# Performance work log

Measured on AMD Instinct MI355X. Metric: run time of the kernel, lower is better.

## Reference

```python
import jax, jax.numpy as jnp
import numpy as np

B, N, H, S = 64, 2048, 128, 8192
K, DEAD_K = 32, 8
BN_EPS = 1e-5


def _bn_train(x, gamma, beta):
    # BatchNorm1d training-mode math over (batch, length) per channel; x: [B,C,N]
    mean = jnp.mean(x, axis=(0, 2), keepdims=True)
    var = jnp.var(x, axis=(0, 2), keepdims=True)
    xh = (x - mean) * jax.lax.rsqrt(var + BN_EPS)
    return xh * gamma[None, :, None] + beta[None, :, None]


def setup_inputs() -> dict:
    key = jax.random.key(0)
    ks = jax.random.split(key, 20)

    def lin(k, out_d, in_d):
        s = 1.0 / np.sqrt(in_d)
        return jax.random.uniform(k, (out_d, in_d), jnp.float32, -s, s)

    def bias(k, d, fan_in):
        s = 1.0 / np.sqrt(fan_in)
        return jax.random.uniform(k, (d,), jnp.float32, -s, s)

    inp = {
        "pts": jax.random.normal(ks[0], (B, 3, N), jnp.float32),
        "dead_features": jax.random.randint(ks[1], (S,), 0, 10, jnp.int32),
        "conv1_w": lin(ks[2], 128, 3), "conv1_b": bias(ks[3], 128, 3),
        "conv2_w": lin(ks[4], 128, 128), "conv2_b": bias(ks[5], 128, 128),
        "conv3_w": lin(ks[6], 256, 128), "conv3_b": bias(ks[7], 256, 128),
        "conv4_w": lin(ks[8], 512, 256), "conv4_b": bias(ks[9], 512, 256),
        "bn1_g": jnp.ones(128), "bn1_b": jnp.zeros(128),
        "bn2_g": jnp.ones(128), "bn2_b": jnp.zeros(128),
        "bn3_g": jnp.ones(256), "bn3_b": jnp.zeros(256),
        "bn4_g": jnp.ones(512), "bn4_b": jnp.zeros(512),
        "fc1_w": lin(ks[10], 256, 512), "fc1_b": bias(ks[11], 256, 512),
        "fc2_w": lin(ks[12], H, 256), "fc2_b": bias(ks[13], H, 256),
        "sae2_w": lin(ks[14], H, S),  # sae1.weight = sae2.weight.T (tied init)
        "sae1_b": jnp.zeros(S), "sae2_b": jnp.zeros(H),
    }
    inp["sae1_w"] = inp["sae2_w"].T  # [S,H]
    return inp


def reference(pts, dead_features, conv1_w, conv1_b, conv2_w, conv2_b,
              conv3_w, conv3_b, conv4_w, conv4_b,
              bn1_g, bn1_b, bn2_g, bn2_b, bn3_g, bn3_b, bn4_g, bn4_b,
              fc1_w, fc1_b, fc2_w, fc2_b, sae2_w, sae1_b, sae2_b, sae1_w):
    def conv1x1(x, w, b):  # x:[B,Ci,N] w:[Co,Ci] -> [B,Co,N]
        return jnp.einsum('bcn,oc->bon', x, w) + b[None, :, None]

    h = jax.nn.relu(_bn_train(conv1x1(pts, conv1_w, conv1_b), bn1_g, bn1_b))
    h = jax.nn.relu(_bn_train(conv1x1(h, conv2_w, conv2_b), bn2_g, bn2_b))
    h = jax.nn.relu(_bn_train(conv1x1(h, conv3_w, conv3_b), bn3_g, bn3_b))
    h = _bn_train(conv1x1(h, conv4_w, conv4_b), bn4_g, bn4_b)
    h = jnp.max(h, axis=2)  # global max pool -> [B,512]
    h = jax.nn.relu(h @ fc1_w.T + fc1_b)
    x = jax.nn.relu(h @ fc2_w.T + fc2_b)  # hidden rep [B,H]

    # run_sae (stage 1, batch_topk=True)
    _x = x - sae2_b
    f = jax.nn.relu(_x @ sae1_w.T + sae1_b)  # [B,S]
    flat = f.reshape(-1)                     # [B*S]
    topk_vals, inds = jax.lax.top_k(flat, K * B)
    dead_mask = jnp.broadcast_to(dead_features >= 5, (B, S)).reshape(-1)
    dead_flat = jnp.where(dead_mask, flat, 0.0)
    dead_vals, dead_inds = jax.lax.top_k(dead_flat, DEAD_K * B)
    f_out = jnp.zeros_like(flat).at[inds].set(topk_vals).reshape(B, S)
    dead_f = jnp.zeros_like(flat).at[dead_inds].set(dead_vals).reshape(B, S)
    recon = f_out @ sae2_w.T + sae2_b
    dead_x = dead_f @ sae2_w.T + sae2_b
    return (x, recon, f_out, dead_x)
```

## Files before the change

kernel.cpp:

```cpp
#include <hip/hip_runtime.h>
#include <hip/hip_bf16.h>
#include <stdint.h>

#define B_   64
#define N_   2048
#define C1_  128
#define C2_  128
#define C3_  256
#define C4_  512
#define H_   128
#define S_   8192
#define KTOT 2048
#define DTOT 512
#define TIE_CAP 4096
#define BN_EPS 1e-5f
#define NPART 1024

#define I_PTS 0
#define I_DEAD 1
#define I_C1W 2
#define I_C1B 3
#define I_C2W 4
#define I_C2B 5
#define I_C3W 6
#define I_C3B 7
#define I_C4W 8
#define I_C4B 9
#define I_BN1G 10
#define I_BN1B 11
#define I_BN2G 12
#define I_BN2B 13
#define I_BN3G 14
#define I_BN3B 15
#define I_BN4G 16
#define I_BN4B 17
#define I_FC1W 18
#define I_FC1B 19
#define I_FC2W 20
#define I_FC2B 21
#define I_SAE2W 22
#define I_SAE1B 23
#define I_SAE2B 24
#define I_SAE1W 25

typedef const void* const* Tbl;
struct P26 { const void* p[26]; };

typedef _Float16 f16x8 __attribute__((ext_vector_type(8)));
typedef float f32x16 __attribute__((ext_vector_type(16)));

typedef const __attribute__((address_space(1))) uint32_t* gas_t;
typedef __attribute__((address_space(3))) uint32_t* las_t;
#define GLL(g, s) __builtin_amdgcn_global_load_lds((gas_t)(const void*)(g), (las_t)(void*)(s), 16, 0, 0)

__global__ void k_sentinel(float* outx, float v){
  if(threadIdx.x==0) outx[0] = v;
}

__global__ void k_route(P26 in, const void** tbl, int* flag){
  if(threadIdx.x != 0) return;
  const uint32_t* a   = (const uint32_t*)in.p[1];
  const uint32_t* g10 = (const uint32_t*)in.p[10];
  const uint32_t* d16 = (const uint32_t*)in.p[16];
  bool onesA  = a[0]==0x3F800000u && a[1]==0x3F800000u && a[2]==0x3F800000u && a[3]==0x3F800000u;
  bool intsA  = a[0]<=9u && a[1]<=9u && a[2]<=9u && a[3]<=9u;
  bool ones10 = g10[0]==0x3F800000u && g10[1]==0x3F800000u;
  bool ints16 = d16[0]<=9u && d16[1]<=9u;
  int f = 0;
  if(intsA && ones10) f = 1;
  else if(onesA && ints16) f = 2;
  const int permI[26] = {0,1,2,3,4,5,6,7,8,9,10,11,12,13,14,15,16,17,18,19,20,21,22,23,24,25};
  const int permA[26] = {21,16,9,8,11,10,13,12,15,14,1,0,3,2,5,4,7,6,18,17,20,19,25,22,24,23};
  const int* pm = (f==2) ? permA : permI;
  for(int i=0;i<26;i++) tbl[i] = in.p[pm[i]];
  *flag = f;
}

__global__ void k_init(uint32_t* ctrl, uint32_t* cnt, uint32_t* hist,
                       uint32_t* ctrl2, uint32_t* cnt2, uint32_t* hist2,
                       float* racc, float* dacc){
  int t = blockIdx.x*256 + threadIdx.x;
  if(t < 256){ hist[t]=0u; hist2[t]=0u; }
  if(t == 0){
    ctrl[0]=0u;  ctrl[1]=KTOT;  cnt[0]=0u;  cnt[1]=0u;  cnt[2]=0u;
    ctrl2[0]=0u; ctrl2[1]=DTOT; cnt2[0]=0u; cnt2[1]=0u; cnt2[2]=0u;
  }
  if(t < B_*H_){ racc[t]=0.f; dacc[t]=0.f; }
}

__global__ void k_mom(Tbl tbl, float* __restrict__ mom){
  const float* pts = (const float*)tbl[I_PTS];
  int b = blockIdx.x, t = threadIdx.x;
  const float* p0 = pts + (size_t)b*3*N_;
  const float* p1 = p0 + N_;
  const float* p2 = p1 + N_;
  float v[9] = {};
  for(int n=t;n<N_;n+=256){
    float a=p0[n], c=p1[n], d=p2[n];
    v[0]+=a; v[1]+=c; v[2]+=d;
    v[3]=fmaf(a,a,v[3]); v[4]=fmaf(a,c,v[4]); v[5]=fmaf(a,d,v[5]);
    v[6]=fmaf(c,c,v[6]); v[7]=fmaf(c,d,v[7]); v[8]=fmaf(d,d,v[8]);
  }
  __shared__ float red[256];
  for(int i=0;i<9;i++){
    red[t]=v[i]; __syncthreads();
    for(int off=128;off>0;off>>=1){ if(t<off) red[t]+=red[t+off]; __syncthreads(); }
    if(t==0) mom[b*16+i]=red[0];
    __syncthreads();
  }
}

__global__ void k_bn1fold(const float* __restrict__ mom, Tbl tbl, float* __restrict__ ew){
  const float* w1 = (const float*)tbl[I_C1W];
  const float* b1 = (const float*)tbl[I_C1B];
  const float* g  = (const float*)tbl[I_BN1G];
  const float* be = (const float*)tbl[I_BN1B];
  __shared__ float tot[9];
  int t = threadIdx.x;
  if(t < 9){
    float s=0.f;
    for(int b=0;b<B_;b++) s += mom[b*16+t];
    tot[t]=s;
  }
  __syncthreads();
  const float inv = 1.f/((float)B_*(float)N_);
  float mu0=tot[0]*inv, mu1=tot[1]*inv, mu2=tot[2]*inv;
  float M00=tot[3]*inv, M01=tot[4]*inv, M02=tot[5]*inv;
  float M11=tot[6]*inv, M12=tot[7]*inv, M22=tot[8]*inv;
  float w0=w1[t*3+0], ww1=w1[t*3+1], w2=w1[t*3+2];
  float bb=b1[t];
  float wmu = w0*mu0 + ww1*mu1 + w2*mu2;
  float m = wmu + bb;
  float E2 = w0*w0*M00 + ww1*ww1*M11 + w2*w2*M22
           + 2.f*(w0*ww1*M01 + w0*w2*M02 + ww1*w2*M12)
           + 2.f*bb*wmu + bb*bb;
  float var = E2 - m*m; if(var<0.f) var=0.f;
  float a = g[t] / sqrtf(var + BN_EPS);
  float sh = be[t] - m*a;
  ew[t*4+0]=a*w0; ew[t*4+1]=a*ww1; ew[t*4+2]=a*w2; ew[t*4+3]=fmaf(a,bb,sh);
}

template<int CI, int CO, int SRCP, int STOREY, int MM, int TILED>
__global__ __launch_bounds__(256)
void k_conv(const float* __restrict__ yin, Tbl tbl, int wi, int bi,
            const float* __restrict__ aAct, const float* __restrict__ bAct,
            float* __restrict__ yout,
            float* __restrict__ psum, float* __restrict__ psq,
            float* __restrict__ pmx, float* __restrict__ pmn){
  const float* W    = (const float*)tbl[wi];
  const float* bias = (const float*)tbl[bi];
  __shared__ float Ws[16][132];
  __shared__ float As[16][132];
  __shared__ float ps[3][128];
  const int b  = blockIdx.z;
  const int o0 = blockIdx.y*128;
  const int n0 = blockIdx.x*128;
  const int nt = blockIdx.x;
  const int t  = threadIdx.x;
  const int tx = t & 15, ty = t >> 4;
  const int wo = t >> 1;
  const int wk = (t & 1)*8;
  const int ar = t >> 4;
  const int an4 = (t & 15)*4;
  if(SRCP){
    const float* pts = (const float*)tbl[I_PTS];
    if(t < 48){
      int j = t >> 4, cc = (t & 15)*8;
      const float* pp = pts + ((size_t)b*3 + j)*N_ + n0 + cc;
      const float4 p0 = *(const float4*)pp;
      const float4 p1 = *(const float4*)(pp+4);
      ps[j][cc+0]=p0.x; ps[j][cc+1]=p0.y; ps[j][cc+2]=p0.z; ps[j][cc+3]=p0.w;
      ps[j][cc+4]=p1.x; ps[j][cc+5]=p1.y; ps[j][cc+6]=p1.z; ps[j][cc+7]=p1.w;
    }
    __syncthreads();
  }
  const float* ybase = SRCP ? (const float*)nullptr : (yin + (size_t)b*CI*N_);
  float acc[8][8] = {};
  for(int k0=0;k0<CI;k0+=16){
    {
      const float* wp = W + (size_t)(o0+wo)*CI + (k0+wk);
      const float4 wa = *(const float4*)wp;
      const float4 wb = *(const float4*)(wp+4);
      Ws[wk+0][wo]=wa.x; Ws[wk+1][wo]=wa.y; Ws[wk+2][wo]=wa.z; Ws[wk+3][wo]=wa.w;
      Ws[wk+4][wo]=wb.x; Ws[wk+5][wo]=wb.y; Ws[wk+6][wo]=wb.z; Ws[wk+7][wo]=wb.w;
    }
    {
      const int c = k0 + ar;
      float av[8];
      if(SRCP){
        const float e0=aAct[c*4+0], e1=aAct[c*4+1], e2=aAct[c*4+2], e3=aAct[c*4+3];
        #pragma unroll
        for(int x=0;x<4;x++){
          float v = fmaf(e0, ps[0][an4+x], fmaf(e1, ps[1][an4+x], fmaf(e2, ps[2][an4+x], e3)));
          av[x] = fmaxf(v, 0.f);
        }
        #pragma unroll
        for(int x=0;x<4;x++){
          float v = fmaf(e0, ps[0][64+an4+x], fmaf(e1, ps[1][64+an4+x], fmaf(e2, ps[2][64+an4+x], e3)));
          av[4+x] = fmaxf(v, 0.f);
        }
      } else {
        const float* yp = ybase + (size_t)c*N_ + n0;
        const float4 v0 = *(const float4*)(yp + an4);
        const float4 v1 = *(const float4*)(yp + 64 + an4);
        const float a = aAct[c], bb = bAct[c];
        av[0]=fmaxf(fmaf(a,v0.x,bb),0.f); av[1]=fmaxf(fmaf(a,v0.y,bb),0.f);
        av[2]=fmaxf(fmaf(a,v0.z,bb),0.f); av[3]=fmaxf(fmaf(a,v0.w,bb),0.f);
        av[4]=fmaxf(fmaf(a,v1.x,bb),0.f); av[5]=fmaxf(fmaf(a,v1.y,bb),0.f);
        av[6]=fmaxf(fmaf(a,v1.z,bb),0.f); av[7]=fmaxf(fmaf(a,v1.w,bb),0.f);
      }
      *(float4*)&As[ar][an4]    = make_float4(av[0],av[1],av[2],av[3]);
      *(float4*)&As[ar][64+an4] = make_float4(av[4],av[5],av[6],av[7]);
    }
    __syncthreads();
    #pragma unroll
    for(int kk=0;kk<16;kk++){
      const float4 w0 = *(const float4*)&Ws[kk][ty*8];
      const float4 w1 = *(const float4*)&Ws[kk][ty*8+4];
      const float4 a0 = *(const float4*)&As[kk][tx*4];
      const float4 a1 = *(const float4*)&As[kk][64+tx*4];
      const float wr[8] = {w0.x,w0.y,w0.z,w0.w,w1.x,w1.y,w1.z,w1.w};
      const float ac[8] = {a0.x,a0.y,a0.z,a0.w,a1.x,a1.y,a1.z,a1.w};
      #pragma unroll
      for(int i=0;i<8;i++)
        #pragma unroll
        for(int j=0;j<8;j++)
          acc[i][j] = fmaf(wr[i], ac[j], acc[i][j]);
    }
    __syncthreads();
  }
  float bo[8];
  #pragma unroll
  for(int i=0;i<8;i++) bo[i] = bias[o0 + ty*8 + i];
  if(STOREY && TILED){
    const int ks = (o0 + ty*8) >> 4;
    float* yb2 = yout + ((((size_t)(b*16 + nt))*16 + ks)*128)*16 + (ty&1)*8;
    #pragma unroll
    for(int jj=0;jj<8;jj++){
      const int nn = (jj<4) ? (tx*4 + jj) : (64 + tx*4 + (jj-4));
      float4 lo = make_float4(acc[0][jj]+bo[0], acc[1][jj]+bo[1],
                              acc[2][jj]+bo[2], acc[3][jj]+bo[3]);
      float4 hi = make_float4(acc[4][jj]+bo[4], acc[5][jj]+bo[5],
                              acc[6][jj]+bo[6], acc[7][jj]+bo[7]);
      *(float4*)(yb2 + (size_t)nn*16)     = lo;
      *(float4*)(yb2 + (size_t)nn*16 + 4) = hi;
    }
  }
  #pragma unroll
  for(int i=0;i<8;i++){
    const int o = o0 + ty*8 + i;
    float v[8];
    #pragma unroll
    for(int j=0;j<8;j++) v[j] = acc[i][j] + bo[i];
    if(STOREY && !TILED){
      float* yo = yout + ((size_t)b*CO + o)*N_ + n0;
      *(float4*)(yo + tx*4)      = make_float4(v[0],v[1],v[2],v[3]);
      *(float4*)(yo + 64 + tx*4) = make_float4(v[4],v[5],v[6],v[7]);
    }
    float s = 0.f, q = 0.f;
    #pragma unroll
    for(int j=0;j<8;j++){ s += v[j]; q = fmaf(v[j],v[j],q); }
    float mx=0.f, mn=0.f;
    if(MM){
      mx = v[0]; mn = v[0];
      #pragma unroll
      for(int j=1;j<8;j++){ mx = fmaxf(mx,v[j]); mn = fminf(mn,v[j]); }
    }
    #pragma unroll
    for(int m=1;m<16;m<<=1){
      s += __shfl_xor(s,m);
      q += __shfl_xor(q,m);
      if(MM){ mx = fmaxf(mx,__shfl_xor(mx,m)); mn = fminf(mn,__shfl_xor(mn,m)); }
    }
    if(tx==0){
      psum[(size_t)o*NPART + b*16 + nt] = s;
      psq [(size_t)o*NPART + b*16 + nt] = q;
      if(MM){
        pmx[((size_t)b*CO + o)*16 + nt] = mx;
        pmn[((size_t)b*CO + o)*16 + nt] = mn;
      }
    }
  }
}

__global__ void k_wcvt(Tbl tbl, _Float16* __restrict__ whi, _Float16* __restrict__ wlo){
  const float* W = (const float*)tbl[I_C4W];
  int u = blockIdx.x*256 + threadIdx.x;
  int h = u & 1, o_loc = (u>>1)&127, ks = (u>>8)&15, oy = u>>12;
  int o = oy*128 + o_loc;
  int c0 = ks*16 + h*8;
  const float* wp = W + (size_t)o*C3_ + c0;
  f16x8 vh, vl;
  #pragma unroll
  for(int j=0;j<8;j++){
    float w = wp[j]*1024.f;
    _Float16 hi = (_Float16)w;
    vh[j] = hi;
    vl[j] = (_Float16)(w - (float)hi);
  }
  *(f16x8*)(whi + (size_t)u*8) = vh;
  *(f16x8*)(wlo + (size_t)u*8) = vl;
}

__global__ void k_t3(const float* __restrict__ y3t, const float* __restrict__ a3,
                     const float* __restrict__ b3, _Float16* __restrict__ a4){
  int u = blockIdx.x*256 + threadIdx.x;
  int h = u & 1, ks = (u>>8)&15;
  int c0 = ks*16 + h*8;
  const float* yp = y3t + (size_t)u*8;
  f16x8 vh;
  #pragma unroll
  for(int j=0;j<8;j++){
    float v = fmaxf(fmaf(a3[c0+j], yp[j], b3[c0+j]), 0.f);
    vh[j] = (_Float16)v;
  }
  *(f16x8*)(a4 + (size_t)u*8) = vh;
}

__global__ __launch_bounds__(256)
void k_conv4m(const _Float16* __restrict__ a4,
              const _Float16* __restrict__ whi, const _Float16* __restrict__ wlo,
              Tbl tbl,
              float* __restrict__ psum, float* __restrict__ psq,
              float* __restrict__ pmx, float* __restrict__ pmn){
  const float* bias = (const float*)tbl[I_C4B];
  __shared__ __align__(16) char smem[73728];
  const int nt = blockIdx.x, oy = blockIdx.y, b = blockIdx.z;
  const int t = threadIdx.x, l = t & 63, w = t >> 6;
  const int wr = w >> 1, wc = w & 1, h = l >> 5, ln = l & 31;
  const char* gWh = (const char*)whi + (size_t)oy*65536;
  const char* gWl = (const char*)wlo + (size_t)oy*65536;
  const char* gA  = (const char*)a4  + (size_t)(b*16 + nt)*65536;
  const int lo16 = l*16;
  const int aoff0 = (wr*64 +  0 + ln)*32 + h*16;
  const int aoff1 = (wr*64 + 32 + ln)*32 + h*16;
  const int boff0 = (wc*64 +  0 + ln)*32 + h*16;
  const int boff1 = (wc*64 + 32 + ln)*32 + h*16;
  f32x16 acc00 = {}, acc01 = {}, acc10 = {}, acc11 = {};

  auto stage = [&](int buf, int step){
    char* sb = smem + buf*24576;
    const size_t go = (size_t)step*8192;
    #pragma unroll
    for(int i=0;i<2;i++){
      const int off = i*4096 + w*1024;
      GLL(gWh + go + off + lo16, sb         + off);
      GLL(gWl + go + off + lo16, sb + 8192  + off);
      GLL(gA  + go + off + lo16, sb + 16384 + off);
    }
  };

  stage(0, 0);
  stage(1, 1);
  #pragma unroll
  for(int s=0; s<8; s++){
    if(s < 7){ asm volatile("s_waitcnt vmcnt(6)" ::: "memory"); }
    else     { asm volatile("s_waitcnt vmcnt(0)" ::: "memory"); }
    __builtin_amdgcn_s_barrier();
    if(s < 6) stage((s+2)%3, s+2);
    const char* sb = smem + (s%3)*24576;
    __builtin_amdgcn_s_setprio(1);
    #pragma unroll
    for(int g=0; g<2; g++){
      const char* pg = sb + g*4096;
      f16x8 ah0 = *(const f16x8*)(pg + aoff0);
      f16x8 ah1 = *(const f16x8*)(pg + aoff1);
      f16x8 al0 = *(const f16x8*)(pg + 8192 + aoff0);
      f16x8 al1 = *(const f16x8*)(pg + 8192 + aoff1);
      f16x8 b0  = *(const f16x8*)(pg + 16384 + boff0);
      f16x8 b1  = *(const f16x8*)(pg + 16384 + boff1);
      acc00 = __builtin_amdgcn_mfma_f32_32x32x16_f16(ah0, b0, acc00, 0,0,0);
      acc00 = __builtin_amdgcn_mfma_f32_32x32x16_f16(al0, b0, acc00, 0,0,0);
      acc01 = __builtin_amdgcn_mfma_f32_32x32x16_f16(ah0, b1, acc01, 0,0,0);
      acc01 = __builtin_amdgcn_mfma_f32_32x32x16_f16(al0, b1, acc01, 0,0,0);
      acc10 = __builtin_amdgcn_mfma_f32_32x32x16_f16(ah1, b0, acc10, 0,0,0);
      acc10 = __builtin_amdgcn_mfma_f32_32x32x16_f16(al1, b0, acc10, 0,0,0);
      acc11 = __builtin_amdgcn_mfma_f32_32x32x16_f16(ah1, b1, acc11, 0,0,0);
      acc11 = __builtin_amdgcn_mfma_f32_32x32x16_f16(al1, b1, acc11, 0,0,0);
    }
    __builtin_amdgcn_s_setprio(0);
  }
  __syncthreads();
  float* Ss = (float*)smem;
  float* Sq = Ss + 1024;
  float* Sx = Sq + 1024;
  float* Sn = Sx + 1024;
  const float inv = 1.f/1024.f;
  const int o0 = oy*128;
  const int grp = ln >> 3;
  #pragma unroll
  for(int to=0; to<2; to++){
    const f32x16 a0 = to ? acc10 : acc00;
    const f32x16 a1 = to ? acc11 : acc01;
    #pragma unroll
    for(int r=0; r<16; r++){
      const int row = (r&3) + 8*(r>>2) + 4*h;
      const int ol = wr*64 + to*32 + row;
      const float bo = bias[o0 + ol];
      float v0 = fmaf(a0[r], inv, bo);
      float v1 = fmaf(a1[r], inv, bo);
      float s = v0 + v1;
      float q = fmaf(v0, v0, v1*v1);
      float mx = fmaxf(v0, v1), mn = fminf(v0, v1);
      #pragma unroll
      for(int m=1; m<8; m<<=1){
        s += __shfl_xor(s, m);
        q += __shfl_xor(q, m);
        mx = fmaxf(mx, __shfl_xor(mx, m));
        mn = fminf(mn, __shfl_xor(mn, m));
      }
      if((ln & 7) == 0){
        const int idx = (wc*4 + grp)*128 + ol;
        Ss[idx] = s;  Sq[idx] = q;
        Sx[idx] = mx; Sn[idx] = mn;
      }
    }
  }
  __syncthreads();
  if(t < 128){
    const int o = o0 + t;
    float s = 0.f, q = 0.f;
    float mx = -__builtin_inff(), mn = __builtin_inff();
    #pragma unroll
    for(int g=0; g<8; g++){
      s += Ss[g*128 + t];
      q += Sq[g*128 + t];
      mx = fmaxf(mx, Sx[g*128 + t]);
      mn = fminf(mn, Sn[g*128 + t]);
    }
    psum[(size_t)o*NPART + b*16 + nt] = s;
    psq [(size_t)o*NPART + b*16 + nt] = q;
    pmx[((size_t)b*C4_ + o)*16 + nt] = mx;
    pmn[((size_t)b*C4_ + o)*16 + nt] = mn;
  }
}

__global__ void k_finalize(const float* __restrict__ psum, const float* __restrict__ psq,
                           Tbl tbl, int gi, int bi,
                           float* __restrict__ aout, float* __restrict__ bout){
  const float* gamma = (const float*)tbl[gi];
  const float* beta  = (const float*)tbl[bi];
  int c = blockIdx.x, t = threadIdx.x;
  float s=0.f, q=0.f;
  for(int i=t;i<NPART;i+=256){ s+=psum[(size_t)c*NPART+i]; q+=psq[(size_t)c*NPART+i]; }
  __shared__ float ls[256], lq[256];
  ls[t]=s; lq[t]=q; __syncthreads();
  for(int off=128; off>0; off>>=1){
    if(t<off){ ls[t]+=ls[t+off]; lq[t]+=lq[t+off]; }
    __syncthreads();
  }
  if(t==0){
    const float cnt = (float)B_*(float)N_;
    float mean = ls[0]/cnt;
    float var  = lq[0]/cnt - mean*mean;
    if(var < 0.f) var = 0.f;
    float a = gamma[c] / sqrtf(var + BN_EPS);
    aout[c] = a;
    bout[c] = beta[c] - mean*a;
  }
}

__global__ void k_pool(const float* __restrict__ pmx, const float* __restrict__ pmn,
                       const float* __restrict__ aA, const float* __restrict__ bA,
                       float* __restrict__ pooled){
  int idx = blockIdx.x*256 + threadIdx.x;
  int o = idx & (C4_-1);
  float mx=-__builtin_inff(), mn=__builtin_inff();
  for(int k=0;k<16;k++){
    mx = fmaxf(mx, pmx[(size_t)idx*16+k]);
    mn = fminf(mn, pmn[(size_t)idx*16+k]);
  }
  float a=aA[o], bb=bA[o];
  pooled[idx] = (a>=0.f) ? fmaf(a,mx,bb) : fmaf(a,mn,bb);
}

__global__ void k_fc1(const float* __restrict__ pooled, Tbl tbl, float* __restrict__ out){
  const float* w    = (const float*)tbl[I_FC1W];
  const float* bias = (const float*)tbl[I_FC1B];
  __shared__ float xp[512];
  int b = blockIdx.x, t = threadIdx.x;
  for(int i=t;i<512;i+=256) xp[i] = pooled[(size_t)b*512+i];
  __syncthreads();
  const float* wr = w + (size_t)t*512;
  float acc = 0.f;
  for(int c=0;c<512;c++) acc = fmaf(xp[c], wr[c], acc);
  out[(size_t)b*256 + t] = fmaxf(acc + bias[t], 0.f);
}

__global__ void k_fc2(const float* __restrict__ in, Tbl tbl,
                      float* __restrict__ xbuf, float* __restrict__ xout){
  const float* w    = (const float*)tbl[I_FC2W];
  const float* bias = (const float*)tbl[I_FC2B];
  __shared__ float xp[256];
  int b = blockIdx.x, t = threadIdx.x;
  for(int i=t;i<256;i+=128) xp[i] = in[(size_t)b*256+i];
  __syncthreads();
  const float* wr = w + (size_t)t*256;
  float acc = 0.f;
  for(int c=0;c<256;c++) acc = fmaf(xp[c], wr[c], acc);
  float v = fmaxf(acc + bias[t], 0.f);
  xbuf[(size_t)b*H_ + t] = v;
  xout[(size_t)b*H_ + t] = v;
}

__global__ void k_sae(const float* __restrict__ xbuf, Tbl tbl, float* __restrict__ f){
  const float* w  = (const float*)tbl[I_SAE1W];
  const float* b1 = (const float*)tbl[I_SAE1B];
  const float* b2 = (const float*)tbl[I_SAE2B];
  __shared__ float xp[H_];
  int b = blockIdx.y, t = threadIdx.x;
  if(t < H_) xp[t] = xbuf[(size_t)b*H_ + t] - b2[t];
  __syncthreads();
  int s = blockIdx.x*256 + t;
  const float* wr = w + (size_t)s*H_;
  float acc = 0.f;
  for(int h=0;h<H_;h++) acc = fmaf(xp[h], wr[h], acc);
  acc += b1[s];
  f[(size_t)b*S_ + s] = fmaxf(acc, 0.f);
}

__global__ void k_hist(const float* __restrict__ f, Tbl tbl,
                       int mode, int shift, const uint32_t* __restrict__ ctrl,
                       uint32_t* __restrict__ hist){
  const int* df = (const int*)tbl[I_DEAD];
  __shared__ uint32_t lh[256];
  int t = threadIdx.x;
  lh[t] = 0u; __syncthreads();
  const uint32_t prefix = ctrl[0];
  const uint32_t mask = (shift == 24) ? 0u : (0xFFFFFFFFu << (shift+8));
  int i0 = blockIdx.x*1024 + t;
  #pragma unroll
  for(int j=0;j<4;j++){
    int i = i0 + j*256;
    float v = f[i];
    if(mode){ int s = i & (S_-1); if(df[s] < 5) v = 0.f; }
    uint32_t u = __float_as_uint(v);
    if((u & mask) == prefix) atomicAdd(&lh[(u>>shift)&255u], 1u);
  }
  __syncthreads();
  if(lh[t]) atomicAdd(&hist[t], lh[t]);
}

__global__ void k_scan(uint32_t* ctrl, uint32_t* hist, int shift){
  if(threadIdx.x == 0){
    uint32_t rem = ctrl[1];
    uint32_t cum = 0; int tb = 0;
    for(int bin=255; bin>=0; bin--){
      uint32_t c = hist[bin];
      if(cum + c >= rem){ tb = bin; rem = rem - cum; break; }
      cum += c;
    }
    ctrl[0] |= ((uint32_t)tb) << shift;
    ctrl[1] = rem;
  }
  __syncthreads();
  hist[threadIdx.x] = 0u;
}

__global__ void k_select(const float* __restrict__ f, Tbl tbl,
                         int mode, int kcap, const uint32_t* __restrict__ ctrl,
                         uint32_t* __restrict__ cnt, uint32_t* __restrict__ sel,
                         uint32_t* __restrict__ tie){
  const int* df = (const int*)tbl[I_DEAD];
  int i = blockIdx.x*256 + threadIdx.x;
  float v = f[i];
  if(mode){ int s = i & (S_-1); if(df[s] < 5) v = 0.f; }
  uint32_t u = __float_as_uint(v);
  const uint32_t T = ctrl[0];
  if(u > T){ uint32_t p = atomicAdd(&cnt[0], 1u); if(p < (uint32_t)kcap) sel[p] = (uint32_t)i; }
  else if(u == T){ uint32_t p = atomicAdd(&cnt[1], 1u); if(p < TIE_CAP) tie[p] = (uint32_t)i; }
}

__global__ void k_resolve(const uint32_t* __restrict__ ctrl, uint32_t* __restrict__ cnt,
                          uint32_t* __restrict__ sel, const uint32_t* __restrict__ tie,
                          int kcap){
  if(threadIdx.x != 0) return;
  uint32_t m = ctrl[1];
  uint32_t ngt = cnt[0]; if(ngt > (uint32_t)kcap) ngt = (uint32_t)kcap;
  uint32_t ntie = cnt[1]; if(ntie > TIE_CAP) ntie = TIE_CAP;
  uint32_t last = 0u; bool first = true;
  for(uint32_t it=0; it<m; it++){
    uint32_t best = 0xFFFFFFFFu;
    for(uint32_t j=0;j<ntie;j++){
      uint32_t v = tie[j];
      if((first || v > last) && v < best) best = v;
    }
    if(best == 0xFFFFFFFFu) break;
    if(ngt + it < (uint32_t)kcap) sel[ngt + it] = best;
    last = best; first = false;
  }
  uint32_t tot = ngt + m; if(tot > (uint32_t)kcap) tot = (uint32_t)kcap;
  cnt[2] = tot;
}

__global__ void k_scatter(const uint32_t* __restrict__ sel, const uint32_t* __restrict__ cnt,
                          const float* __restrict__ f, float* __restrict__ fout){
  uint32_t t = blockIdx.x*256 + threadIdx.x;
  if(t >= cnt[2]) return;
  uint32_t i = sel[t];
  if(i < (uint32_t)(B_*S_)) fout[i] = f[i];
}

__global__ void k_accum(const uint32_t* __restrict__ sel, const uint32_t* __restrict__ cnt,
                        const float* __restrict__ f, Tbl tbl, int mode,
                        float* __restrict__ acc){
  const int* df = (const int*)tbl[I_DEAD];
  const float* w2 = (const float*)tbl[I_SAE2W];
  uint32_t e = blockIdx.x;
  if(e >= cnt[2]) return;
  uint32_t i = sel[e];
  if(i >= (uint32_t)(B_*S_)) return;
  uint32_t b = i >> 13, s = i & (S_-1);
  float v = f[i];
  if(mode && df[s] < 5) v = 0.f;
  int h = threadIdx.x;
  float wv = w2[(size_t)h*S_ + s];
  atomicAdd(&acc[b*H_ + h], v*wv);
}

__global__ void k_final(const float* __restrict__ racc, const float* __restrict__ dacc,
                        Tbl tbl, float* __restrict__ outR, float* __restrict__ outD){
  const float* b2 = (const float*)tbl[I_SAE2B];
  int idx = blockIdx.x*256 + threadIdx.x;
  int h = idx & (H_-1);
  float bb = b2[h];
  outR[idx] = racc[idx] + bb;
  outD[idx] = dacc[idx] + bb;
}

__global__ void k_health(const int* __restrict__ flag, const float* __restrict__ xb,
                         float* __restrict__ outx){
  __shared__ float red[256];
  int t = threadIdx.x;
  float s = 0.f;
  for(int i=t;i<B_*H_;i+=256) s += fabsf(xb[i]);
  red[t]=s; __syncthreads();
  for(int off=128;off>0;off>>=1){ if(t<off) red[t]+=red[t+off]; __syncthreads(); }
  if(t==0){
    float avg = red[0]/(float)(B_*H_);
    int f = *flag;
    float v = 0.f;
    if(f == 0) v = 12000.f;
    else if(!(avg >= 0.05f && avg <= 50.f)) v = 40000.f + 1000.f*(float)f;
    if(v > 0.f) outx[0] = v;
  }
}

extern "C" void kernel_launch(void* const* d_in, const int* in_sizes, int n_in,
                              void* d_out, int out_size, void* d_ws, size_t ws_size,
                              hipStream_t stream){
  (void)in_sizes; (void)n_in;
  float* out       = (float*)d_out;
  float* out_x     = out;
  float* out_recon = out + 8192;
  float* out_fout  = out + 16384;
  float* out_deadx = out + 540672;

  char* p = (char*)d_ws;
  auto take = [&](size_t bytes)->char*{
    char* r = p; p += (bytes + 255) & ~(size_t)255; return r;
  };
  float* y2   = (float*)take((size_t)B_*C2_*N_*4);
  float* y3   = (float*)take((size_t)B_*C3_*N_*4);
  float* psum = (float*)take((size_t)C4_*NPART*4);
  float* psq  = (float*)take((size_t)C4_*NPART*4);
  float* pmx  = (float*)take((size_t)B_*C4_*16*4);
  float* pmn  = (float*)take((size_t)B_*C4_*16*4);
  float* mom  = (float*)take(64*16*4);
  float* ab   = (float*)take(4096*4);
  float* pooled=(float*)take((size_t)B_*C4_*4);
  float* fc1o = (float*)take((size_t)B_*256*4);
  float* xb   = (float*)take((size_t)B_*H_*4);
  float* fb   = (float*)take((size_t)B_*S_*4);
  float* racc = (float*)take((size_t)B_*H_*4);
  float* dacc = (float*)take((size_t)B_*H_*4);
  uint32_t* hist  = (uint32_t*)take(256*4);
  uint32_t* ctrl  = (uint32_t*)take(64);
  uint32_t* cnt   = (uint32_t*)take(64);
  uint32_t* sel   = (uint32_t*)take((size_t)KTOT*4);
  uint32_t* tie   = (uint32_t*)take((size_t)TIE_CAP*4);
  uint32_t* hist2 = (uint32_t*)take(256*4);
  uint32_t* ctrl2 = (uint32_t*)take(64);
  uint32_t* cnt2  = (uint32_t*)take(64);
  uint32_t* sel2  = (uint32_t*)take((size_t)DTOT*4);
  uint32_t* tie2  = (uint32_t*)take((size_t)TIE_CAP*4);
  const void** tbl = (const void**)take(32*sizeof(void*));
  int* flag = (int*)take(64);
  size_t need = (size_t)(p - (char*)d_ws);
  _Float16* a4   = (_Float16*)y2;
  _Float16* w4hi = (_Float16*)fb;
  _Float16* w4lo = (_Float16*)((char*)fb + 262144);

  hipMemsetAsync(d_out, 0, (size_t)out_size*sizeof(float), stream);
  if(ws_size != 0 && ws_size < need){
    k_sentinel<<<1,64,0,stream>>>(out_x, 15000.f);
    return;
  }

  P26 ptrs;
  for(int i=0;i<26;i++) ptrs.p[i] = d_in[i];
  k_route<<<1,64,0,stream>>>(ptrs, tbl, flag);
  k_init<<<32,256,0,stream>>>(ctrl,cnt,hist,ctrl2,cnt2,hist2,racc,dacc);

  k_mom<<<B_,256,0,stream>>>(tbl,mom);
  k_bn1fold<<<1,128,0,stream>>>(mom,tbl,ab);
  k_wcvt<<<64,256,0,stream>>>(tbl, w4hi, w4lo);

  k_conv<C1_,C2_,1,1,0,0><<<dim3(N_/128,C2_/128,B_),256,0,stream>>>(
      nullptr,tbl,I_C2W,I_C2B,ab,nullptr,y2,psum,psq,nullptr,nullptr);
  k_finalize<<<C2_,256,0,stream>>>(psum,psq,tbl,I_BN2G,I_BN2B,ab+512,ab+640);
  k_conv<C2_,C3_,0,1,0,1><<<dim3(N_/128,C3_/128,B_),256,0,stream>>>(
      y2,tbl,I_C3W,I_C3B,ab+512,ab+640,y3,psum,psq,nullptr,nullptr);
  k_finalize<<<C3_,256,0,stream>>>(psum,psq,tbl,I_BN3G,I_BN3B,ab+768,ab+1024);
  k_t3<<<16384,256,0,stream>>>(y3, ab+768, ab+1024, a4);
  k_conv4m<<<dim3(16,4,64),256,0,stream>>>(a4, w4hi, w4lo, tbl,
                                           psum, psq, pmx, pmn);
  k_finalize<<<C4_,256,0,stream>>>(psum,psq,tbl,I_BN4G,I_BN4B,ab+1280,ab+1792);
  k_pool<<<(B_*C4_)/256,256,0,stream>>>(pmx,pmn,ab+1280,ab+1792,pooled);

  k_fc1<<<B_,256,0,stream>>>(pooled,tbl,fc1o);
  k_fc2<<<B_,128,0,stream>>>(fc1o,tbl,xb,out_x);
  k_sae<<<dim3(S_/256,B_),256,0,stream>>>(xb,tbl,fb);

  for(int pass=0;pass<4;pass++){
    int shift = 24 - 8*pass;
    k_hist<<<512,256,0,stream>>>(fb,tbl,0,shift,ctrl,hist);
    k_scan<<<1,256,0,stream>>>(ctrl,hist,shift);
  }
  k_select<<<2048,256,0,stream>>>(fb,tbl,0,KTOT,ctrl,cnt,sel,tie);
  k_resolve<<<1,64,0,stream>>>(ctrl,cnt,sel,tie,KTOT);
  k_scatter<<<8,256,0,stream>>>(sel,cnt,fb,out_fout);
  k_accum<<<KTOT,128,0,stream>>>(sel,cnt,fb,tbl,0,racc);

  for(int pass=0;pass<4;pass++){
    int shift = 24 - 8*pass;
    k_hist<<<512,256,0,stream>>>(fb,tbl,1,shift,ctrl2,hist2);
    k_scan<<<1,256,0,stream>>>(ctrl2,hist2,shift);
  }
  k_select<<<2048,256,0,stream>>>(fb,tbl,1,DTOT,ctrl2,cnt2,sel2,tie2);
  k_resolve<<<1,64,0,stream>>>(ctrl2,cnt2,sel2,tie2,DTOT);
  k_accum<<<DTOT,128,0,stream>>>(sel2,cnt2,fb,tbl,1,dacc);

  k_final<<<(B_*H_)/256,256,0,stream>>>(racc,dacc,tbl,out_recon,out_deadx);

  k_health<<<1,256,0,stream>>>(flag,xb,out_x);
}
```

Measured before the change: 718.0 us.

## Load conv4 MFMA fragments directly from global with fragment-ordered operand layouts

The weight-split and activation-transform kernels now write their f16 outputs in an MFMA-fragment order, so each lane's 16-byte operand is contiguous and coalesced in global memory. The conv4 GEMM drops the triple-buffered LDS staging (global_load_lds, waitcnt and barriers) and instead reads fragments straight into registers, prefetching one k-step ahead. This removes LDS traffic and block-wide synchronisation from the main loop and shrinks shared memory, which may allow higher occupancy. In exchange, operands that two waves used to share through LDS are now fetched separately by each wave from global/L2, and there is only one step of latency hiding.

New measurement: 686.8 us. 1.05x faster.

```diff
diff --git a/kernel.cpp b/kernel.cpp
--- a/kernel.cpp
+++ b/kernel.cpp
@@ -48,10 +48,6 @@
 
 typedef _Float16 f16x8 __attribute__((ext_vector_type(8)));
 typedef float f32x16 __attribute__((ext_vector_type(16)));
-
-typedef const __attribute__((address_space(1))) uint32_t* gas_t;
-typedef __attribute__((address_space(3))) uint32_t* las_t;
-#define GLL(g, s) __builtin_amdgcn_global_load_lds((gas_t)(const void*)(g), (las_t)(void*)(s), 16, 0, 0)
 
 __global__ void k_sentinel(float* outx, float v){
   if(threadIdx.x==0) outx[0] = v;
@@ -298,14 +294,15 @@
     vh[j] = hi;
     vl[j] = (_Float16)(w - (float)hi);
   }
-  *(f16x8*)(whi + (size_t)u*8) = vh;
-  *(f16x8*)(wlo + (size_t)u*8) = vl;
+  int uo = (oy*16 + ks)*256 + (o_loc>>5)*64 + h*32 + (o_loc&31);
+  *(f16x8*)(whi + (size_t)uo*8) = vh;
+  *(f16x8*)(wlo + (size_t)uo*8) = vl;
 }
 
 __global__ void k_t3(const float* __restrict__ y3t, const float* __restrict__ a3,
                      const float* __restrict__ b3, _Float16* __restrict__ a4){
   int u = blockIdx.x*256 + threadIdx.x;
-  int h = u & 1, ks = (u>>8)&15;
+  int h = u & 1, nn = (u>>1)&127, ks = (u>>8)&15, tile = u>>12;
   int c0 = ks*16 + h*8;
   const float* yp = y3t + (size_t)u*8;
   f16x8 vh;
@@ -314,7 +311,8 @@
     float v = fmaxf(fmaf(a3[c0+j], yp[j], b3[c0+j]), 0.f);
     vh[j] = (_Float16)v;
   }
-  *(f16x8*)(a4 + (size_t)u*8) = vh;
+  int uo = (tile*16 + ks)*256 + (nn>>5)*64 + h*32 + (nn&31);
+  *(f16x8*)(a4 + (size_t)uo*8) = vh;
 }
 
 __global__ __launch_bounds__(256)
@@ -324,64 +322,43 @@
               float* __restrict__ psum, float* __restrict__ psq,
               float* __restrict__ pmx, float* __restrict__ pmn){
   const float* bias = (const float*)tbl[I_C4B];
-  __shared__ __align__(16) char smem[73728];
+  __shared__ float sred[4096];
   const int nt = blockIdx.x, oy = blockIdx.y, b = blockIdx.z;
   const int t = threadIdx.x, l = t & 63, w = t >> 6;
   const int wr = w >> 1, wc = w & 1, h = l >> 5, ln = l & 31;
-  const char* gWh = (const char*)whi + (size_t)oy*65536;
-  const char* gWl = (const char*)wlo + (size_t)oy*65536;
-  const char* gA  = (const char*)a4  + (size_t)(b*16 + nt)*65536;
-  const int lo16 = l*16;
-  const int aoff0 = (wr*64 +  0 + ln)*32 + h*16;
-  const int aoff1 = (wr*64 + 32 + ln)*32 + h*16;
-  const int boff0 = (wc*64 +  0 + ln)*32 + h*16;
-  const int boff1 = (wc*64 + 32 + ln)*32 + h*16;
+  const char* gWh = (const char*)whi + (size_t)oy*65536 + wr*2048 + l*16;
+  const char* gWl = (const char*)wlo + (size_t)oy*65536 + wr*2048 + l*16;
+  const char* gA  = (const char*)a4  + (size_t)(b*16 + nt)*65536 + wc*2048 + l*16;
   f32x16 acc00 = {}, acc01 = {}, acc10 = {}, acc11 = {};
-
-  auto stage = [&](int buf, int step){
-    char* sb = smem + buf*24576;
-    const size_t go = (size_t)step*8192;
-    #pragma unroll
-    for(int i=0;i<2;i++){
-      const int off = i*4096 + w*1024;
-      GLL(gWh + go + off + lo16, sb         + off);
-      GLL(gWl + go + off + lo16, sb + 8192  + off);
-      GLL(gA  + go + off + lo16, sb + 16384 + off);
-    }
-  };
-
-  stage(0, 0);
-  stage(1, 1);
+  f16x8 nah0 = *(const f16x8*)(gWh);
+  f16x8 nah1 = *(const f16x8*)(gWh + 1024);
+  f16x8 nal0 = *(const f16x8*)(gWl);
+  f16x8 nal1 = *(const f16x8*)(gWl + 1024);
+  f16x8 nb0  = *(const f16x8*)(gA);
+  f16x8 nb1  = *(const f16x8*)(gA + 1024);
   #pragma unroll
-  for(int s=0; s<8; s++){
-    if(s < 7){ asm volatile("s_waitcnt vmcnt(6)" ::: "memory"); }
-    else     { asm volatile("s_waitcnt vmcnt(0)" ::: "memory"); }
-    __builtin_amdgcn_s_barrier();
-    if(s < 6) stage((s+2)%3, s+2);
-    const char* sb = smem + (s%3)*24576;
-    __builtin_amdgcn_s_setprio(1);
-    #pragma unroll
-    for(int g=0; g<2; g++){
-      const char* pg = sb + g*4096;
-      f16x8 ah0 = *(const f16x8*)(pg + aoff0);
-      f16x8 ah1 = *(const f16x8*)(pg + aoff1);
-      f16x8 al0 = *(const f16x8*)(pg + 8192 + aoff0);
-      f16x8 al1 = *(const f16x8*)(pg + 8192 + aoff1);
-      f16x8 b0  = *(const f16x8*)(pg + 16384 + boff0);
-      f16x8 b1  = *(const f16x8*)(pg + 16384 + boff1);
-      acc00 = __builtin_amdgcn_mfma_f32_32x32x16_f16(ah0, b0, acc00, 0,0,0);
-      acc00 = __builtin_amdgcn_mfma_f32_32x32x16_f16(al0, b0, acc00, 0,0,0);
-      acc01 = __builtin_amdgcn_mfma_f32_32x32x16_f16(ah0, b1, acc01, 0,0,0);
-      acc01 = __builtin_amdgcn_mfma_f32_32x32x16_f16(al0, b1, acc01, 0,0,0);
-      acc10 = __builtin_amdgcn_mfma_f32_32x32x16_f16(ah1, b0, acc10, 0,0,0);
-      acc10 = __builtin_amdgcn_mfma_f32_32x32x16_f16(al1, b0, acc10, 0,0,0);
-      acc11 = __builtin_amdgcn_mfma_f32_32x32x16_f16(ah1, b1, acc11, 0,0,0);
-      acc11 = __builtin_amdgcn_mfma_f32_32x32x16_f16(al1, b1, acc11, 0,0,0);
-    }
-    __builtin_amdgcn_s_setprio(0);
-  }
-  __syncthreads();
-  float* Ss = (float*)smem;
+  for(int ks=0; ks<16; ks++){
+    f16x8 ah0 = nah0, ah1 = nah1, al0 = nal0, al1 = nal1;
+    f16x8 b0  = nb0,  b1  = nb1;
+    if(ks < 15){
+      const int o = (ks+1)*4096;
+      nah0 = *(const f16x8*)(gWh + o);
+      nah1 = *(const f16x8*)(gWh + o + 1024);
+      nal0 = *(const f16x8*)(gWl + o);
+      nal1 = *(const f16x8*)(gWl + o + 1024);
+      nb0  = *(const f16x8*)(gA  + o);
+      nb1  = *(const f16x8*)(gA  + o + 1024);
+    }
+    acc00 = __builtin_amdgcn_mfma_f32_32x32x16_f16(ah0, b0, acc00, 0,0,0);
+    acc00 = __builtin_amdgcn_mfma_f32_32x32x16_f16(al0, b0, acc00, 0,0,0);
+    acc01 = __builtin_amdgcn_mfma_f32_32x32x16_f16(ah0, b1, acc01, 0,0,0);
+    acc01 = __builtin_amdgcn_mfma_f32_32x32x16_f16(al0, b1, acc01, 0,0,0);
+    acc10 = __builtin_amdgcn_mfma_f32_32x32x16_f16(ah1, b0, acc10, 0,0,0);
+    acc10 = __builtin_amdgcn_mfma_f32_32x32x16_f16(al1, b0, acc10, 0,0,0);
+    acc11 = __builtin_amdgcn_mfma_f32_32x32x16_f16(ah1, b1, acc11, 0,0,0);
+    acc11 = __builtin_amdgcn_mfma_f32_32x32x16_f16(al1, b1, acc11, 0,0,0);
+  }
+  float* Ss = sred;
   float* Sq = Ss + 1024;
   float* Sx = Sq + 1024;
   float* Sn = Sx + 1024;
```
